# Kernel tuning notes

Hardware: AMD Instinct MI355X
Metric: run time of the kernel (lower is better)

The kernel has to match this reference:

```python
import jax, jax.numpy as jnp
import numpy as np

IN_F = 4096
OUT_F = 4096
NNZ = 1638400
TOKENS = 8192


def setup_inputs() -> dict:
    key = jax.random.key(0)
    k1, k2, k3, k4, k5 = jax.random.split(key, 5)
    x = jax.random.normal(k1, (TOKENS, IN_F), dtype=jnp.float32)
    weight_pruned = jax.random.normal(k2, (NNZ,), dtype=jnp.float32)
    bias = jax.random.normal(k3, (OUT_F,), dtype=jnp.float32)
    row_idx = jax.random.randint(k4, (NNZ,), 0, OUT_F, dtype=jnp.int32)
    col_idx = jax.random.randint(k5, (NNZ,), 0, IN_F, dtype=jnp.int32)
    return {"x": x, "weight_pruned": weight_pruned, "bias": bias,
            "row_idx": row_idx, "col_idx": col_idx}


def reference(x, weight_pruned, bias, row_idx, col_idx):
    # matching torch advanced-index assignment), then dense linear.
    W = jnp.zeros((OUT_F, IN_F), dtype=weight_pruned.dtype)
    W = W.at[row_idx, col_idx].set(weight_pruned)
    return x @ W.T + bias
```

## Files before the change

### kernel.cpp

```cpp
#include <hip/hip_runtime.h>
#include <hip/hip_bf16.h>
#include <cstdint>

#define TOKENS 8192
#define IN_F 4096
#define OUT_F 4096

typedef __bf16 bf16x8 __attribute__((ext_vector_type(8)));
typedef float f32x4 __attribute__((ext_vector_type(4)));

__global__ void scatter_max_kernel(const int* __restrict__ row,
                                   const int* __restrict__ col,
                                   int* __restrict__ M, int nnz) {
    int i = blockIdx.x * blockDim.x + threadIdx.x;
    if (i < nnz) {
        atomicMax(&M[row[i] * IN_F + col[i]], i);
    }
}

__global__ void scatter_write_kernel(const int* __restrict__ row,
                                     const int* __restrict__ col,
                                     const float* __restrict__ w,
                                     const int* __restrict__ M,
                                     __bf16* __restrict__ Wb, int nnz) {
    int i = blockIdx.x * blockDim.x + threadIdx.x;
    if (i < nnz) {
        int cell = row[i] * IN_F + col[i];
        if (M[cell] == i) Wb[cell] = (__bf16)w[i];
    }
}

__global__ void convert_x_kernel(const float* __restrict__ x,
                                 __bf16* __restrict__ xb) {
    int i = (blockIdx.x * blockDim.x + threadIdx.x) * 8;
    float4 v0 = *(const float4*)(x + i);
    float4 v1 = *(const float4*)(x + i + 4);
    bf16x8 o;
    o[0] = (__bf16)v0.x; o[1] = (__bf16)v0.y;
    o[2] = (__bf16)v0.z; o[3] = (__bf16)v0.w;
    o[4] = (__bf16)v1.x; o[5] = (__bf16)v1.y;
    o[6] = (__bf16)v1.z; o[7] = (__bf16)v1.w;
    *(bf16x8*)(xb + i) = o;
}

__global__ __launch_bounds__(256) void gemm_bt_kernel(
    const __bf16* __restrict__ A,
    const __bf16* __restrict__ B,
    const float* __restrict__ bias,
    float* __restrict__ C) {
    __shared__ __bf16 As[128 * 32];
    __shared__ __bf16 Bs[128 * 32];

    const int tid  = threadIdx.x;
    const int lane = tid & 63;
    const int wid  = tid >> 6;
    const int m0 = blockIdx.y * 128;
    const int n0 = blockIdx.x * 128;
    const int wm = (wid >> 1) * 64;
    const int wn = (wid & 1) * 64;

    const int srow = lane >> 2;
    const int scol = (lane & 3) * 8;
    const int c0 = wid * 2, c1 = wid * 2 + 1;

    const __bf16* ga0 = A + (size_t)(m0 + c0 * 16 + srow) * IN_F + scol;
    const __bf16* ga1 = A + (size_t)(m0 + c1 * 16 + srow) * IN_F + scol;
    const __bf16* gb0 = B + (size_t)(n0 + c0 * 16 + srow) * IN_F + scol;
    const __bf16* gb1 = B + (size_t)(n0 + c1 * 16 + srow) * IN_F + scol;

    __bf16* la0 = &As[c0 * 512];
    __bf16* la1 = &As[c1 * 512];
    __bf16* lb0 = &Bs[c0 * 512];
    __bf16* lb1 = &Bs[c1 * 512];

    const int fm = lane & 15;
    const int fq = (lane >> 4) * 8;
    const __bf16* fa = &As[(wm + fm) * 32 + fq];
    const __bf16* fb = &Bs[(wn + fm) * 32 + fq];

    f32x4 acc[4][4] = {};

    for (int kt = 0; kt < IN_F; kt += 32) {
        __builtin_amdgcn_global_load_lds(
            (unsigned int __attribute__((address_space(1)))*)(ga0 + kt),
            (unsigned int __attribute__((address_space(3)))*)la0, 16, 0, 0);
        __builtin_amdgcn_global_load_lds(
            (unsigned int __attribute__((address_space(1)))*)(ga1 + kt),
            (unsigned int __attribute__((address_space(3)))*)la1, 16, 0, 0);
        __builtin_amdgcn_global_load_lds(
            (unsigned int __attribute__((address_space(1)))*)(gb0 + kt),
            (unsigned int __attribute__((address_space(3)))*)lb0, 16, 0, 0);
        __builtin_amdgcn_global_load_lds(
            (unsigned int __attribute__((address_space(1)))*)(gb1 + kt),
            (unsigned int __attribute__((address_space(3)))*)lb1, 16, 0, 0);

        __syncthreads();

        bf16x8 afrag[4], bfrag[4];
#pragma unroll
        for (int t = 0; t < 4; ++t) afrag[t] = *(const bf16x8*)(fa + t * 512);
#pragma unroll
        for (int t = 0; t < 4; ++t) bfrag[t] = *(const bf16x8*)(fb + t * 512);

#pragma unroll
        for (int mt = 0; mt < 4; ++mt)
#pragma unroll
            for (int nt = 0; nt < 4; ++nt)
                acc[mt][nt] = __builtin_amdgcn_mfma_f32_16x16x32_bf16(
                    afrag[mt], bfrag[nt], acc[mt][nt], 0, 0, 0);

        __syncthreads();
    }

    float bv[4];
#pragma unroll
    for (int nt = 0; nt < 4; ++nt) bv[nt] = bias[n0 + wn + nt * 16 + fm];
    const int r0 = m0 + wm + (lane >> 4) * 4;
#pragma unroll
    for (int mt = 0; mt < 4; ++mt)
#pragma unroll
        for (int nt = 0; nt < 4; ++nt) {
            const int cc = n0 + wn + nt * 16 + fm;
#pragma unroll
            for (int i = 0; i < 4; ++i) {
                C[(size_t)(r0 + mt * 16 + i) * OUT_F + cc] = acc[mt][nt][i] + bv[nt];
            }
        }
}

extern "C" void kernel_launch(void* const* d_in, const int* in_sizes, int n_in,
                              void* d_out, int out_size, void* d_ws, size_t ws_size,
                              hipStream_t stream) {
    const float* x    = (const float*)d_in[0];
    const float* w    = (const float*)d_in[1];
    const float* bias = (const float*)d_in[2];
    const int*   row  = (const int*)d_in[3];
    const int*   col  = (const int*)d_in[4];
    float* out = (float*)d_out;
    const int nnz = in_sizes[3];

    __bf16* xb = (__bf16*)d_ws;
    __bf16* Wb = (__bf16*)((char*)d_ws + (size_t)TOKENS * IN_F * 2);
    int* M = (int*)d_out;

    hipMemsetAsync(Wb, 0, (size_t)OUT_F * IN_F * 2, stream);
    hipMemsetAsync(M, 0xFF, (size_t)OUT_F * IN_F * 4, stream);

    int sblocks = (nnz + 255) / 256;
    scatter_max_kernel<<<sblocks, 256, 0, stream>>>(row, col, M, nnz);
    scatter_write_kernel<<<sblocks, 256, 0, stream>>>(row, col, w, M, Wb, nnz);

    convert_x_kernel<<<(TOKENS * IN_F / 8 + 255) / 256, 256, 0, stream>>>(x, xb);

    dim3 grid(OUT_F / 128, TOKENS / 128);
    gemm_bt_kernel<<<grid, 256, 0, stream>>>(xb, Wb, bias, out);
}
```

Baseline: 662.4 us.

## Pack index and bf16 weight into 64-bit atomicMax, fuse extract with x conversion

Replaces the two-pass scatter (atomicMax on the index, then a conditional write) with a single pass that atomically maxes a 64-bit word holding the nnz index in the high bits and the bf16 weight bits in the low bits. A dense extract pass then pulls the low 16 bits into the bf16 weight matrix, and that pass is fused into the same launch as the x fp32-to-bf16 conversion. This drops one scatter pass, one memset and one launch. In exchange it uses 64-bit atomics and a dense 128MB buffer that must be zeroed and re-read, where the old code zeroed 64MB for the index map plus 32MB for the bf16 weights.

```diff
diff --git a/kernel.cpp b/kernel.cpp
--- a/kernel.cpp
+++ b/kernel.cpp
@@ -9,38 +9,49 @@
 typedef __bf16 bf16x8 __attribute__((ext_vector_type(8)));
 typedef float f32x4 __attribute__((ext_vector_type(4)));
 
-__global__ void scatter_max_kernel(const int* __restrict__ row,
-                                   const int* __restrict__ col,
-                                   int* __restrict__ M, int nnz) {
+__global__ void scatter_pack_kernel(const int* __restrict__ row,
+                                    const int* __restrict__ col,
+                                    const float* __restrict__ w,
+                                    unsigned long long* __restrict__ P,
+                                    int nnz) {
     int i = blockIdx.x * blockDim.x + threadIdx.x;
     if (i < nnz) {
-        atomicMax(&M[row[i] * IN_F + col[i]], i);
+        __bf16 b = (__bf16)w[i];
+        unsigned short bits;
+        __builtin_memcpy(&bits, &b, 2);
+        unsigned long long pack =
+            ((unsigned long long)(unsigned)i << 16) | (unsigned long long)bits;
+        atomicMax(&P[(size_t)row[i] * IN_F + col[i]], pack);
     }
 }
 
-__global__ void scatter_write_kernel(const int* __restrict__ row,
-                                     const int* __restrict__ col,
-                                     const float* __restrict__ w,
-                                     const int* __restrict__ M,
-                                     __bf16* __restrict__ Wb, int nnz) {
-    int i = blockIdx.x * blockDim.x + threadIdx.x;
-    if (i < nnz) {
-        int cell = row[i] * IN_F + col[i];
-        if (M[cell] == i) Wb[cell] = (__bf16)w[i];
+__global__ void extract_convert_kernel(const unsigned long long* __restrict__ P,
+                                       __bf16* __restrict__ Wb,
+                                       const float* __restrict__ x,
+                                       __bf16* __restrict__ xb,
+                                       int eb) {
+    if ((int)blockIdx.x < eb) {
+        size_t base = ((size_t)blockIdx.x * 256 + threadIdx.x) * 8;
+        bf16x8 o;
+#pragma unroll
+        for (int j = 0; j < 8; ++j) {
+            unsigned short bits = (unsigned short)(P[base + j] & 0xFFFFull);
+            __bf16 b;
+            __builtin_memcpy(&b, &bits, 2);
+            o[j] = b;
+        }
+        *(bf16x8*)(Wb + base) = o;
+    } else {
+        size_t base = ((size_t)(blockIdx.x - eb) * 256 + threadIdx.x) * 8;
+        float4 v0 = *(const float4*)(x + base);
+        float4 v1 = *(const float4*)(x + base + 4);
+        bf16x8 o;
+        o[0] = (__bf16)v0.x; o[1] = (__bf16)v0.y;
+        o[2] = (__bf16)v0.z; o[3] = (__bf16)v0.w;
+        o[4] = (__bf16)v1.x; o[5] = (__bf16)v1.y;
+        o[6] = (__bf16)v1.z; o[7] = (__bf16)v1.w;
+        *(bf16x8*)(xb + base) = o;
     }
-}
-
-__global__ void convert_x_kernel(const float* __restrict__ x,
-                                 __bf16* __restrict__ xb) {
-    int i = (blockIdx.x * blockDim.x + threadIdx.x) * 8;
-    float4 v0 = *(const float4*)(x + i);
-    float4 v1 = *(const float4*)(x + i + 4);
-    bf16x8 o;
-    o[0] = (__bf16)v0.x; o[1] = (__bf16)v0.y;
-    o[2] = (__bf16)v0.z; o[3] = (__bf16)v0.w;
-    o[4] = (__bf16)v1.x; o[5] = (__bf16)v1.y;
-    o[6] = (__bf16)v1.z; o[7] = (__bf16)v1.w;
-    *(bf16x8*)(xb + i) = o;
 }
 
 __global__ __launch_bounds__(256) void gemm_bt_kernel(
@@ -141,16 +152,15 @@
 
     __bf16* xb = (__bf16*)d_ws;
     __bf16* Wb = (__bf16*)((char*)d_ws + (size_t)TOKENS * IN_F * 2);
-    int* M = (int*)d_out;
+    unsigned long long* P = (unsigned long long*)d_out;
 
-    hipMemsetAsync(Wb, 0, (size_t)OUT_F * IN_F * 2, stream);
-    hipMemsetAsync(M, 0xFF, (size_t)OUT_F * IN_F * 4, stream);
+    hipMemsetAsync(P, 0, (size_t)OUT_F * IN_F * 8, stream);
 
-    int sblocks = (nnz + 255) / 256;
-    scatter_max_kernel<<<sblocks, 256, 0, stream>>>(row, col, M, nnz);
-    scatter_write_kernel<<<sblocks, 256, 0, stream>>>(row, col, w, M, Wb, nnz);
+    scatter_pack_kernel<<<(nnz + 255) / 256, 256, 0, stream>>>(row, col, w, P, nnz);
 
-    convert_x_kernel<<<(TOKENS * IN_F / 8 + 255) / 256, 256, 0, stream>>>(x, xb);
+    const int eb = OUT_F * IN_F / (256 * 8);
+    const int cb = TOKENS * IN_F / (256 * 8);
+    extract_convert_kernel<<<eb + cb, 256, 0, stream>>>(P, Wb, x, xb, eb);
 
     dim3 grid(OUT_F / 128, TOKENS / 128);
     gemm_bt_kernel<<<grid, 256, 0, stream>>>(xb, Wb, bias, out);
```

Measured after the change: 634.1 us. 4.3% less time.
